# Performance work log

Hardware: AMD Instinct MI355X
Metric: run time of the kernel (lower is better)

The kernel has to match this reference:

```python
import jax, jax.numpy as jnp
import numpy as np

H = 8  # attention_heads


def _ln(x, w, b, eps=1e-5):
    mu = x.mean(axis=-1, keepdims=True)
    var = x.var(axis=-1, keepdims=True)
    return (x - mu) / jnp.sqrt(var + eps) * w + b


def setup_inputs() -> dict:
    key = jax.random.key(0)
    ks = jax.random.split(key, 10)
    B, T, C, U, D, P = 4, 256, 2048, 4, 512, 512
    s = 0.02
    inp = {
        "model_embed": jax.random.normal(ks[0], (B, T, D), jnp.float32),
        "context_embed_key": jax.random.normal(ks[1], (C, U, D), jnp.float32),
        "context_embed_value": jax.random.normal(ks[2], (C, D), jnp.float32),
        "ln1_w": jnp.ones((D,), jnp.float32), "ln1_b": jnp.zeros((D,), jnp.float32),
        "ln2_w": jnp.ones((D,), jnp.float32), "ln2_b": jnp.zeros((D,), jnp.float32),
        "ln3_w": jnp.ones((D,), jnp.float32), "ln3_b": jnp.zeros((D,), jnp.float32),
        "ln4_w": jnp.ones((D,), jnp.float32), "ln4_b": jnp.zeros((D,), jnp.float32),
        "wq": jax.random.normal(ks[3], (D, D), jnp.float32) * s, "bq": jnp.zeros((D,), jnp.float32),
        "wk": jax.random.normal(ks[4], (D, D), jnp.float32) * s, "bk": jnp.zeros((D,), jnp.float32),
        "wv": jax.random.normal(ks[5], (D, D), jnp.float32) * s, "bv": jnp.zeros((D,), jnp.float32),
        "wo": jax.random.normal(ks[6], (D, D), jnp.float32) * s, "bo": jnp.zeros((D,), jnp.float32),
        "wp": jax.random.normal(ks[7], (D, P), jnp.float32) * s, "bp": jnp.zeros((P,), jnp.float32),
    }
    return inp


def reference(model_embed, context_embed_key, context_embed_value,
              ln1_w, ln1_b, ln2_w, ln2_b, ln3_w, ln3_b, ln4_w, ln4_b,
              wq, bq, wk, bk, wv, bv, wo, bo, wp, bp):
    B, T, D = model_embed.shape
    C, U, _ = context_embed_key.shape
    dk = D // H
    # pre-attention LayerNorms (norm_before_x1/x2/x3)
    q = _ln(model_embed, ln1_w, ln1_b)
    k = _ln(context_embed_key, ln2_w, ln2_b)
    v = _ln(context_embed_value, ln3_w, ln3_b)
    # q/k/v projections, split heads
    q = (q @ wq + bq).reshape(B, T, H, dk)
    k = (k @ wk + bk).reshape(C, U, H, dk)
    v = (v @ wv + bv).reshape(C, H, dk)
    # ColBERT late interaction: score every query token against every
    # context vector, MaxSim over the U vectors of each context entry.
    scores = jnp.einsum('bthd,cuhd->bhtcu', q, k) / jnp.sqrt(jnp.asarray(dk, q.dtype))
    scores = scores.max(axis=-1)                 # [B,H,T,C]
    attn = jax.nn.softmax(scores, axis=-1)       # softmax over contexts C
    out = jnp.einsum('bhtc,chd->bthd', attn, v).reshape(B, T, D)
    out = out @ wo + bo                          # attention output proj
    out = _ln(out, ln4_w, ln4_b)                 # norm_after
    return out @ wp + bp                         # final proj -> [B,T,P]
```

## Files before the change

### kernel.cpp

```cpp
#include <hip/hip_runtime.h>
#include <hip/hip_bf16.h>

using bf16 = __hip_bfloat16;

#define D_DIM 512
#define C_DIM 2048
#define U_DIM 4
#define DK 64

typedef __attribute__((ext_vector_type(8))) short short8;
typedef __attribute__((ext_vector_type(8))) unsigned short ushort8;
typedef __attribute__((ext_vector_type(4))) float f32x4;

__device__ __forceinline__ float dload(const void* p, size_t i, int f) {
    return f ? ((const float*)p)[i] : __bfloat162float(((const bf16*)p)[i]);
}
__device__ __forceinline__ unsigned f2bf(float x) {
    bf16 b = __float2bfloat16(x);
    return (unsigned)*(unsigned short*)&b;
}
__device__ __forceinline__ float bf2f(unsigned short us) {
    unsigned u = ((unsigned)us) << 16;
    return __builtin_bit_cast(float, u);
}

__device__ __forceinline__ int block_detect(const void* __restrict__ x) {
    __shared__ int sred[4];
    const bf16* xb = (const bf16*)x;
    int tid = threadIdx.x;
    int cnt = 0;
    #pragma unroll
    for (int i = 0; i < 4; ++i) {
        ushort8 a = *(const ushort8*)(xb + (size_t)(i * 256 + tid) * 8);
        #pragma unroll
        for (int j = 0; j < 8; ++j) {
            float v = fabsf(bf2f(a[j]));
            if (!(v <= 100.0f)) cnt++;
        }
    }
    #pragma unroll
    for (int o = 32; o > 0; o >>= 1) cnt += __shfl_down(cnt, o);
    if ((tid & 63) == 0) sred[tid >> 6] = cnt;
    __syncthreads();
    int c = sred[0] + sred[1] + sred[2] + sred[3];
    return (c > 400) ? 1 : 0;
}

template <bool LN, bool XF, bool WF>
__device__ __forceinline__ void pack_a_body(const void* __restrict__ X,
                                            const void* __restrict__ lnw,
                                            const void* __restrict__ lnb,
                                            uint4* __restrict__ Af, int tt) {
    int m = threadIdx.x >> 4;
    int kbL = threadIdx.x & 15;
    int row = tt * 16 + m;
    float v[32];
    float s = 0.0f, ss = 0.0f;
    #pragma unroll
    for (int i = 0; i < 4; ++i) {
        int k0 = (kbL + i * 16) * 8;
        if constexpr (XF) {
            const float4* p = (const float4*)((const float*)X + (size_t)row * D_DIM + k0);
            float4 a = p[0], b = p[1];
            v[i*8+0] = a.x; v[i*8+1] = a.y; v[i*8+2] = a.z; v[i*8+3] = a.w;
            v[i*8+4] = b.x; v[i*8+5] = b.y; v[i*8+6] = b.z; v[i*8+7] = b.w;
        } else {
            ushort8 a = *(const ushort8*)((const bf16*)X + (size_t)row * D_DIM + k0);
            #pragma unroll
            for (int j = 0; j < 8; ++j) v[i*8+j] = bf2f(a[j]);
        }
        #pragma unroll
        for (int j = 0; j < 8; ++j) { float x = v[i*8+j]; s += x; ss += x * x; }
    }
    float mu = 0.0f, rs = 1.0f;
    if (LN) {
        #pragma unroll
        for (int o = 1; o < 16; o <<= 1) { s += __shfl_xor(s, o); ss += __shfl_xor(ss, o); }
        mu = s * (1.0f / D_DIM);
        float var = ss * (1.0f / D_DIM) - mu * mu;
        rs = rsqrtf(var + 1e-5f);
    }
    #pragma unroll
    for (int i = 0; i < 4; ++i) {
        int kb = kbL + i * 16;
        int k0 = kb * 8;
        float lw[8], lb[8];
        if (LN) {
            if constexpr (WF) {
                const float4* pw = (const float4*)((const float*)lnw + k0);
                const float4* pb = (const float4*)((const float*)lnb + k0);
                float4 w0 = pw[0], w1 = pw[1], b0 = pb[0], b1 = pb[1];
                lw[0]=w0.x; lw[1]=w0.y; lw[2]=w0.z; lw[3]=w0.w;
                lw[4]=w1.x; lw[5]=w1.y; lw[6]=w1.z; lw[7]=w1.w;
                lb[0]=b0.x; lb[1]=b0.y; lb[2]=b0.z; lb[3]=b0.w;
                lb[4]=b1.x; lb[5]=b1.y; lb[6]=b1.z; lb[7]=b1.w;
            } else {
                ushort8 w8 = *(const ushort8*)((const bf16*)lnw + k0);
                ushort8 b8 = *(const ushort8*)((const bf16*)lnb + k0);
                #pragma unroll
                for (int j = 0; j < 8; ++j) { lw[j] = bf2f(w8[j]); lb[j] = bf2f(b8[j]); }
            }
        }
        unsigned pk[4];
        #pragma unroll
        for (int jp = 0; jp < 4; ++jp) {
            float v0 = v[i * 8 + jp * 2];
            float v1 = v[i * 8 + jp * 2 + 1];
            if (LN) {
                v0 = (v0 - mu) * rs * lw[jp * 2] + lb[jp * 2];
                v1 = (v1 - mu) * rs * lw[jp * 2 + 1] + lb[jp * 2 + 1];
            }
            pk[jp] = f2bf(v0) | (f2bf(v1) << 16);
        }
        uint4 wv = {pk[0], pk[1], pk[2], pk[3]};
        Af[((size_t)tt * 64 + kb) * 16 + m] = wv;
    }
}

template <bool WF>
__device__ __forceinline__ void pack_w_body(const void* __restrict__ W,
                                            uint4* __restrict__ Bf, int b,
                                            float (*t)[65]) {
    int n0 = (b & 7) * 64, k0 = (b >> 3) * 64;
    int tid = threadIdx.x;
    if constexpr (WF) {
        #pragma unroll
        for (int i = 0; i < 4; ++i) {
            int e = i * 256 + tid;
            int r = e >> 4, c = (e & 15) * 4;
            float4 a = *(const float4*)((const float*)W + (size_t)(k0 + r) * D_DIM + n0 + c);
            t[r][c] = a.x; t[r][c+1] = a.y; t[r][c+2] = a.z; t[r][c+3] = a.w;
        }
    } else {
        #pragma unroll
        for (int i = 0; i < 2; ++i) {
            int e = i * 256 + tid;
            int r = e >> 3, c = (e & 7) * 8;
            ushort8 a = *(const ushort8*)((const bf16*)W + (size_t)(k0 + r) * D_DIM + n0 + c);
            #pragma unroll
            for (int j = 0; j < 8; ++j) t[r][c + j] = bf2f(a[j]);
        }
    }
    __syncthreads();
    #pragma unroll
    for (int i = 0; i < 2; ++i) {
        int e = i * 256 + tid;
        int nl = e & 63, kbl = e >> 6;
        unsigned pk[4];
        #pragma unroll
        for (int jp = 0; jp < 4; ++jp)
            pk[jp] = f2bf(t[kbl * 8 + jp * 2][nl]) | (f2bf(t[kbl * 8 + jp * 2 + 1][nl]) << 16);
        uint4 wv = {pk[0], pk[1], pk[2], pk[3]};
        int n = n0 + nl;
        Bf[(((size_t)(n >> 4)) * 64 + (k0 / 8 + kbl)) * 16 + (n & 15)] = wv;
    }
}

__global__ __launch_bounds__(256, 1)
void pack_all_kernel(const void* __restrict__ me, const void* __restrict__ l1w, const void* __restrict__ l1b,
                     const void* __restrict__ ck, const void* __restrict__ l2w, const void* __restrict__ l2b,
                     const void* __restrict__ cv, const void* __restrict__ l3w, const void* __restrict__ l3b,
                     uint4* __restrict__ Aq, uint4* __restrict__ Ak, uint4* __restrict__ Av,
                     const void* W0, const void* W1, const void* W2,
                     const void* W3, const void* W4,
                     uint4* B0, uint4* B1, uint4* B2, uint4* B3, uint4* B4,
                     int* __restrict__ flagp) {
    __shared__ float t[64][65];
    int f = block_detect(me);
    if (blockIdx.x == 0 && threadIdx.x == 0) *flagp = f;
    int b = blockIdx.x;
    const void* Ws[5] = {W0, W1, W2, W3, W4};
    uint4* Bs[5] = {B0, B1, B2, B3, B4};
    if (f) {
        if (b < 64)       pack_a_body<true, true, true>(me, l1w, l1b, Aq, b);
        else if (b < 576) pack_a_body<true, true, true>(ck, l2w, l2b, Ak, b - 64);
        else if (b < 704) pack_a_body<true, true, true>(cv, l3w, l3b, Av, b - 576);
        else { int c = b - 704; pack_w_body<true>(Ws[c >> 6], Bs[c >> 6], c & 63, t); }
    } else {
        if (b < 64)       pack_a_body<true, false, false>(me, l1w, l1b, Aq, b);
        else if (b < 576) pack_a_body<true, false, false>(ck, l2w, l2b, Ak, b - 64);
        else if (b < 704) pack_a_body<true, false, false>(cv, l3w, l3b, Av, b - 576);
        else { int c = b - 704; pack_w_body<false>(Ws[c >> 6], Bs[c >> 6], c & 63, t); }
    }
}

template <int OUT>
__device__ __forceinline__ void mfma_gemm_body(const uint4* __restrict__ Af,
                                               const uint4* __restrict__ Bf,
                                               const void* __restrict__ bias,
                                               uint4* __restrict__ Fout, int Rtt,
                                               int f, int bx, int by,
                                               float (*t)[65]) {
    int w = threadIdx.x >> 6, lane = threadIdx.x & 63;
    int q = lane >> 4, mn = lane & 15;
    int mt = by * 4 + w;
    int nt0 = bx * 4;
    f32x4 acc[4] = {{0.f,0.f,0.f,0.f},{0.f,0.f,0.f,0.f},{0.f,0.f,0.f,0.f},{0.f,0.f,0.f,0.f}};
    for (int kw = 0; kw < 16; ++kw) {
        short8 a = *(const short8*)(Af + ((size_t)mt * 64 + kw * 4 + q) * 16 + mn);
        #pragma unroll
        for (int i = 0; i < 4; ++i) {
            short8 b = *(const short8*)(Bf + (((size_t)(nt0 + i)) * 64 + kw * 4 + q) * 16 + mn);
            acc[i] = __builtin_amdgcn_mfma_f32_16x16x32_bf16(a, b, acc[i], 0, 0, 0);
        }
    }
    #pragma unroll
    for (int i = 0; i < 4; ++i) {
        float bv = dload(bias, (nt0 + i) * 16 + mn, f);
        #pragma unroll
        for (int r = 0; r < 4; ++r)
            t[w * 16 + q * 4 + r][i * 16 + mn] = acc[i][r] + bv;
    }
    __syncthreads();
    int h = bx;
    if constexpr (OUT == 1) {
        #pragma unroll
        for (int e0 = 0; e0 < 2; ++e0) {
            int e = e0 * 256 + threadIdx.x;
            int m = e & 15, kb = (e >> 4) & 7, ttl = e >> 7;
            const float* src = &t[ttl * 16 + m][kb * 8];
            uint4 wv;
            wv.x = f2bf(src[0]) | (f2bf(src[1]) << 16);
            wv.y = f2bf(src[2]) | (f2bf(src[3]) << 16);
            wv.z = f2bf(src[4]) | (f2bf(src[5]) << 16);
            wv.w = f2bf(src[6]) | (f2bf(src[7]) << 16);
            Fout[(((size_t)h * Rtt + by * 4 + ttl) * 8 + kb) * 16 + m] = wv;
        }
    } else if constexpr (OUT == 2) {
        #pragma unroll
        for (int e0 = 0; e0 < 2; ++e0) {
            int e = e0 * 256 + threadIdx.x;
            int lane2 = e & 63, nt = (e >> 6) & 3, ctl = e >> 8;
            int nm2 = lane2 & 15, q2 = lane2 >> 4;
            int col = nt * 16 + nm2;
            int rb = ctl * 32 + q2 * 8;
            uint4 wv;
            wv.x = f2bf(t[rb + 0][col]) | (f2bf(t[rb + 1][col]) << 16);
            wv.y = f2bf(t[rb + 2][col]) | (f2bf(t[rb + 3][col]) << 16);
            wv.z = f2bf(t[rb + 4][col]) | (f2bf(t[rb + 5][col]) << 16);
            wv.w = f2bf(t[rb + 6][col]) | (f2bf(t[rb + 7][col]) << 16);
            Fout[(((size_t)h * 64 + by * 2 + ctl) * 4 + nt) * 64 + lane2] = wv;
        }
    } else {
        #pragma unroll
        for (int e0 = 0; e0 < 2; ++e0) {
            int e = e0 * 256 + threadIdx.x;
            int m2 = e & 15, kb = (e >> 4) & 7, u = e >> 7;
            const float* src = &t[m2 * 4 + u][kb * 8];
            uint4 wv;
            wv.x = f2bf(src[0]) | (f2bf(src[1]) << 16);
            wv.y = f2bf(src[2]) | (f2bf(src[3]) << 16);
            wv.z = f2bf(src[4]) | (f2bf(src[5]) << 16);
            wv.w = f2bf(src[6]) | (f2bf(src[7]) << 16);
            int nt = by * 4 + u;
            Fout[(((size_t)h * 512 + nt) * 8 + kb) * 16 + m2] = wv;
        }
    }
}

__global__ __launch_bounds__(256, 1)
void gemm_qkv_kernel(const uint4* __restrict__ Aq, const uint4* __restrict__ Ak,
                     const uint4* __restrict__ Av,
                     const uint4* __restrict__ wfq, const uint4* __restrict__ wfk,
                     const uint4* __restrict__ wfv,
                     const void* __restrict__ bq, const void* __restrict__ bk,
                     const void* __restrict__ bv,
                     uint4* __restrict__ qf, uint4* __restrict__ kf,
                     uint4* __restrict__ vf,
                     const int* __restrict__ flagp) {
    __shared__ float t[64][65];
    int f = *flagp;
    int b = blockIdx.x;
    if (b < 1024) {
        mfma_gemm_body<3>(Ak, wfk, bk, kf, 512, f, b >> 7, b & 127, t);
    } else if (b < 1280) {
        int c = b - 1024;
        mfma_gemm_body<2>(Av, wfv, bv, vf, 0, f, c >> 5, c & 31, t);
    } else {
        int c = b - 1280;
        mfma_gemm_body<1>(Aq, wfq, bq, qf, 64, f, c >> 4, c & 15, t);
    }
}

__global__ __launch_bounds__(256, 1)
void attn_fused_kernel(const uint4* __restrict__ qf, const uint4* __restrict__ kf,
                       const uint4* __restrict__ vf,
                       float* __restrict__ pacc, float* __restrict__ pm,
                       float* __restrict__ pl) {
    __shared__ float sp[4][16][36];
    int tid = threadIdx.x;
    int w = tid >> 6, lane = tid & 63;
    int q = lane >> 4, nm = lane & 15;
    int b = blockIdx.x;
    int h = b & 7;
    int s = (b >> 3) & 7;
    int qb = b >> 6;
    int mt = qb * 4 + w;

    short8 a0 = *(const short8*)(qf + (((size_t)h * 64 + mt) * 8 + q) * 16 + nm);
    short8 a1 = *(const short8*)(qf + (((size_t)h * 64 + mt) * 8 + 4 + q) * 16 + nm);

    f32x4 sc[8][2];
    #pragma unroll
    for (int st = 0; st < 8; ++st) {
        #pragma unroll
        for (int hh = 0; hh < 2; ++hh) {
            int ct16 = (s * 8 + st) * 2 + hh;
            f32x4 scv = {-1e30f, -1e30f, -1e30f, -1e30f};
            __builtin_amdgcn_s_setprio(1);
            #pragma unroll
            for (int u = 0; u < 4; ++u) {
                int nt = ct16 * 4 + u;
                short8 b0 = *(const short8*)(kf + (((size_t)h * 512 + nt) * 8 + q) * 16 + nm);
                short8 b1 = *(const short8*)(kf + (((size_t)h * 512 + nt) * 8 + 4 + q) * 16 + nm);
                f32x4 acc = {0.0f, 0.0f, 0.0f, 0.0f};
                acc = __builtin_amdgcn_mfma_f32_16x16x32_bf16(a0, b0, acc, 0, 0, 0);
                acc = __builtin_amdgcn_mfma_f32_16x16x32_bf16(a1, b1, acc, 0, 0, 0);
                #pragma unroll
                for (int r = 0; r < 4; ++r) scv[r] = fmaxf(scv[r], acc[r]);
            }
            __builtin_amdgcn_s_setprio(0);
            #pragma unroll
            for (int r = 0; r < 4; ++r) sc[st][hh][r] = scv[r] * 0.125f;
        }
    }

    float mrow[4], lrow[4];
    #pragma unroll
    for (int r = 0; r < 4; ++r) {
        float m = sc[0][0][r];
        #pragma unroll
        for (int st = 0; st < 8; ++st) {
            m = fmaxf(m, sc[st][0][r]);
            m = fmaxf(m, sc[st][1][r]);
        }
        m = fmaxf(m, __shfl_xor(m, 1));
        m = fmaxf(m, __shfl_xor(m, 2));
        m = fmaxf(m, __shfl_xor(m, 4));
        m = fmaxf(m, __shfl_xor(m, 8));
        mrow[r] = m;
        lrow[r] = 0.0f;
    }

    f32x4 acc_o[4] = {{0.f,0.f,0.f,0.f},{0.f,0.f,0.f,0.f},{0.f,0.f,0.f,0.f},{0.f,0.f,0.f,0.f}};
    #pragma unroll
    for (int st = 0; st < 8; ++st) {
        #pragma unroll
        for (int r = 0; r < 4; ++r) {
            float p0 = __expf(sc[st][0][r] - mrow[r]);
            float p1 = __expf(sc[st][1][r] - mrow[r]);
            sp[w][q * 4 + r][nm] = p0;
            sp[w][q * 4 + r][16 + nm] = p1;
            lrow[r] += p0 + p1;
        }
        float4 pa0 = *(const float4*)&sp[w][nm][q * 8];
        float4 pa1 = *(const float4*)&sp[w][nm][q * 8 + 4];
        uint4 av;
        av.x = f2bf(pa0.x) | (f2bf(pa0.y) << 16);
        av.y = f2bf(pa0.z) | (f2bf(pa0.w) << 16);
        av.z = f2bf(pa1.x) | (f2bf(pa1.y) << 16);
        av.w = f2bf(pa1.z) | (f2bf(pa1.w) << 16);
        short8 ap = *(short8*)&av;
        int ct32 = s * 8 + st;
        __builtin_amdgcn_s_setprio(1);
        #pragma unroll
        for (int nt2 = 0; nt2 < 4; ++nt2) {
            short8 bv = *(const short8*)(vf + (((size_t)h * 64 + ct32) * 4 + nt2) * 64 + lane);
            acc_o[nt2] = __builtin_amdgcn_mfma_f32_16x16x32_bf16(ap, bv, acc_o[nt2], 0, 0, 0);
        }
        __builtin_amdgcn_s_setprio(0);
    }

    #pragma unroll
    for (int r = 0; r < 4; ++r) {
        float ps = lrow[r];
        ps += __shfl_xor(ps, 1);
        ps += __shfl_xor(ps, 2);
        ps += __shfl_xor(ps, 4);
        ps += __shfl_xor(ps, 8);
        lrow[r] = ps;
    }

    int p_idx = ((qb * 8 + h) << 3) + s;
    float* po = pacc + ((size_t)p_idx * 64 + w * 16) * 64;
    #pragma unroll
    for (int nt2 = 0; nt2 < 4; ++nt2)
        #pragma unroll
        for (int r = 0; r < 4; ++r)
            po[(q * 4 + r) * 64 + nt2 * 16 + nm] = acc_o[nt2][r];
    if (nm == 0) {
        #pragma unroll
        for (int r = 0; r < 4; ++r) {
            pm[p_idx * 64 + w * 16 + q * 4 + r] = mrow[r];
            pl[p_idx * 64 + w * 16 + q * 4 + r] = lrow[r];
        }
    }
}

__global__ __launch_bounds__(256, 1)
void attn_merge_kernel(const float* __restrict__ pacc, const float* __restrict__ pm,
                       const float* __restrict__ pl, uint4* __restrict__ oAf) {
    int b = blockIdx.x;
    int g = b >> 1;
    int qb = g >> 3, h = g & 7;
    int tid = threadIdx.x;
    int r32 = tid >> 3, dg = tid & 7;
    int t_loc = (b & 1) * 32 + r32;
    int p0 = g * 8;
    float M = -1e30f;
    #pragma unroll
    for (int s = 0; s < 8; ++s) M = fmaxf(M, pm[(p0 + s) * 64 + t_loc]);
    float L = 0.0f;
    float4 o0 = {}, o1 = {};
    #pragma unroll
    for (int s = 0; s < 8; ++s) {
        float e = __expf(pm[(p0 + s) * 64 + t_loc] - M);
        L += pl[(p0 + s) * 64 + t_loc] * e;
        const float4* po = (const float4*)(pacc + ((size_t)(p0 + s) * 64 + t_loc) * 64 + dg * 8);
        float4 v0 = po[0], v1 = po[1];
        o0.x += v0.x * e; o0.y += v0.y * e; o0.z += v0.z * e; o0.w += v0.w * e;
        o1.x += v1.x * e; o1.y += v1.y * e; o1.z += v1.z * e; o1.w += v1.w * e;
    }
    float inv = 1.0f / L;
    int t = qb * 64 + t_loc;
    int tt = t >> 4, m = t & 15;
    int kb = h * 8 + dg;
    uint4 u;
    u.x = f2bf(o0.x * inv) | (f2bf(o0.y * inv) << 16);
    u.y = f2bf(o0.z * inv) | (f2bf(o0.w * inv) << 16);
    u.z = f2bf(o1.x * inv) | (f2bf(o1.y * inv) << 16);
    u.w = f2bf(o1.z * inv) | (f2bf(o1.w * inv) << 16);
    oAf[((size_t)tt * 64 + kb) * 16 + m] = u;
}

__global__ __launch_bounds__(512, 1)
void tail2_kernel(const uint4* __restrict__ oAf,
                  const uint4* __restrict__ wfo, const uint4* __restrict__ wfp,
                  const void* __restrict__ bo, const void* __restrict__ bp,
                  const void* __restrict__ ln4w, const void* __restrict__ ln4b,
                  float* __restrict__ Y, const int* __restrict__ flagp) {
    __shared__ uint4 lfr[64][16];
    __shared__ float xs[8][16][68];
    __shared__ float lw4[512], lb4[512];
    __shared__ float sred[8][16][2];
    int f = *flagp;
    int tid = threadIdx.x;
    int rt = blockIdx.x;
    if (tid < 512) { lw4[tid] = dload(ln4w, tid, f); lb4[tid] = dload(ln4b, tid, f); }

    int w = tid >> 6, lane = tid & 63;
    int q = lane >> 4, mn = lane & 15;

    f32x4 acc[4] = {{0.f,0.f,0.f,0.f},{0.f,0.f,0.f,0.f},{0.f,0.f,0.f,0.f},{0.f,0.f,0.f,0.f}};
    for (int kw = 0; kw < 16; ++kw) {
        short8 a = *(const short8*)(oAf + ((size_t)rt * 64 + kw * 4 + q) * 16 + mn);
        #pragma unroll
        for (int i = 0; i < 4; ++i) {
            int nt = w * 4 + i;
            short8 b = *(const short8*)(wfo + ((size_t)nt * 64 + kw * 4 + q) * 16 + mn);
            acc[i] = __builtin_amdgcn_mfma_f32_16x16x32_bf16(a, b, acc[i], 0, 0, 0);
        }
    }
    #pragma unroll
    for (int i = 0; i < 4; ++i) {
        float bv = dload(bo, (w * 4 + i) * 16 + mn, f);
        #pragma unroll
        for (int r = 0; r < 4; ++r) acc[i][r] += bv;
    }

    {
        float ps[4], pq[4];
        #pragma unroll
        for (int r = 0; r < 4; ++r) {
            float s = 0.f, sq = 0.f;
            #pragma unroll
            for (int i = 0; i < 4; ++i) { float x = acc[i][r]; s += x; sq += x * x; }
            #pragma unroll
            for (int o = 1; o < 16; o <<= 1) { s += __shfl_xor(s, o); sq += __shfl_xor(sq, o); }
            ps[r] = s; pq[r] = sq;
        }
        if (mn == 0) {
            #pragma unroll
            for (int r = 0; r < 4; ++r) { sred[w][q*4+r][0] = ps[r]; sred[w][q*4+r][1] = pq[r]; }
        }
    }
    __syncthreads();

    float mu[4], rs[4];
    #pragma unroll
    for (int r = 0; r < 4; ++r) {
        int rr = q * 4 + r;
        float s = 0.f, sq = 0.f;
        #pragma unroll
        for (int ww = 0; ww < 8; ++ww) { s += sred[ww][rr][0]; sq += sred[ww][rr][1]; }
        mu[r] = s * (1.0f / D_DIM);
        float var = sq * (1.0f / D_DIM) - mu[r] * mu[r];
        rs[r] = rsqrtf(var + 1e-5f);
    }

    #pragma unroll
    for (int i = 0; i < 4; ++i) {
        int col = w * 64 + i * 16 + mn;
        float g = lw4[col], bb = lb4[col];
        #pragma unroll
        for (int r = 0; r < 4; ++r) {
            float x = (acc[i][r] - mu[r]) * rs[r] * g + bb;
            xs[w][q * 4 + r][i * 16 + mn] = x;
        }
    }
    __syncthreads();

    #pragma unroll
    for (int it = 0; it < 2; ++it) {
        int idx = it * 64 + lane;
        int m = idx & 15, kbl = idx >> 4;
        const float* src = &xs[w][m][kbl * 8];
        float4 s0 = *(const float4*)src;
        float4 s1 = *(const float4*)(src + 4);
        uint4 u;
        u.x = f2bf(s0.x) | (f2bf(s0.y) << 16);
        u.y = f2bf(s0.z) | (f2bf(s0.w) << 16);
        u.z = f2bf(s1.x) | (f2bf(s1.y) << 16);
        u.w = f2bf(s1.z) | (f2bf(s1.w) << 16);
        lfr[w * 8 + kbl][m] = u;
    }
    __syncthreads();

    f32x4 acc2[4] = {{0.f,0.f,0.f,0.f},{0.f,0.f,0.f,0.f},{0.f,0.f,0.f,0.f},{0.f,0.f,0.f,0.f}};
    for (int kw = 0; kw < 16; ++kw) {
        short8 a = *(const short8*)&lfr[kw * 4 + q][mn];
        #pragma unroll
        for (int i = 0; i < 4; ++i) {
            int nt = w * 4 + i;
            short8 b = *(const short8*)(wfp + ((size_t)nt * 64 + kw * 4 + q) * 16 + mn);
            acc2[i] = __builtin_amdgcn_mfma_f32_16x16x32_bf16(a, b, acc2[i], 0, 0, 0);
        }
    }
    #pragma unroll
    for (int i = 0; i < 4; ++i) {
        int col = (w * 4 + i) * 16 + mn;
        float bv = dload(bp, col, f);
        #pragma unroll
        for (int r = 0; r < 4; ++r)
            Y[(size_t)(rt * 16 + q * 4 + r) * D_DIM + col] = acc2[i][r] + bv;
    }
}

extern "C" void kernel_launch(void* const* d_in, const int* in_sizes, int n_in,
                              void* d_out, int out_size, void* d_ws, size_t ws_size,
                              hipStream_t stream) {
    const void* model_embed = d_in[0];
    const void* ctx_key     = d_in[1];
    const void* ctx_val     = d_in[2];
    const void* ln1w = d_in[3];  const void* ln1b = d_in[4];
    const void* ln2w = d_in[5];  const void* ln2b = d_in[6];
    const void* ln3w = d_in[7];  const void* ln3b = d_in[8];
    const void* ln4w = d_in[9];  const void* ln4b = d_in[10];
    const void* wq = d_in[11];   const void* bq = d_in[12];
    const void* wk = d_in[13];   const void* bk = d_in[14];
    const void* wv = d_in[15];   const void* bv = d_in[16];
    const void* wo = d_in[17];   const void* bo = d_in[18];
    const void* wp = d_in[19];   const void* bp = d_in[20];

    int*   flagp = (int*)d_ws;
    float* ws    = (float*)d_ws + 16;
    float* o1    = ws;
    float* qTf   = o1 + 524288;
    float* kTf   = qTf + 262144;
    float* Aqf   = kTf + 2097152;
    float* Akf   = Aqf + 262144;
    float* Avf   = Akf + 2097152;
    float* vff   = Avf + 524288;
    float* pacc2 = vff + 524288;
    float* pm2   = pacc2 + 4194304;
    float* pl2   = pm2 + 65536;
    float* wfr   = pl2 + 65536;

    uint4* qf  = (uint4*)qTf;
    uint4* kf  = (uint4*)kTf;
    uint4* Aq  = (uint4*)Aqf;
    uint4* Ak  = (uint4*)Akf;
    uint4* Av  = (uint4*)Avf;
    uint4* vf  = (uint4*)vff;
    uint4* oAf = (uint4*)o1;
    uint4* wfq = (uint4*)wfr;
    uint4* wfk = wfq + 32768;
    uint4* wfv = wfk + 32768;
    uint4* wfo = wfv + 32768;
    uint4* wfp = wfo + 32768;

    pack_all_kernel<<<1024, 256, 0, stream>>>(model_embed, ln1w, ln1b,
                                              ctx_key, ln2w, ln2b,
                                              ctx_val, ln3w, ln3b,
                                              Aq, Ak, Av,
                                              wq, wk, wv, wo, wp,
                                              wfq, wfk, wfv, wfo, wfp, flagp);

    gemm_qkv_kernel<<<1408, 256, 0, stream>>>(Aq, Ak, Av, wfq, wfk, wfv,
                                              bq, bk, bv, qf, kf, vf, flagp);

    attn_fused_kernel<<<1024, 256, 0, stream>>>(qf, kf, vf, pacc2, pm2, pl2);

    attn_merge_kernel<<<256, 256, 0, stream>>>(pacc2, pm2, pl2, oAf);

    tail2_kernel<<<64, 512, 0, stream>>>(oAf, wfo, wfp, bo, bp,
                                         ln4w, ln4b, (float*)d_out, flagp);

    (void)ws_size;
}
```

Baseline: 185.9 us.

## Fuse split-context attention merge into attention kernel via shared memory

Each attention block now holds 8 waves, one per context split, working on a single 16-row query tile for one head. Partial outputs and softmax statistics go to LDS instead of global memory, and the block merges them before writing the bf16 result. This removes the separate merge kernel launch and a large global round trip of partial accumulators. In exchange, each block covers fewer query rows, so K/V reuse across query tiles inside a block is lost, and most threads sit idle during the merge. Separately, the QKV GEMM launch bound is raised to allow two blocks per CU.

Measured after the change: 182.2 us. 1.02x faster.

```diff
diff --git a/kernel.cpp b/kernel.cpp
--- a/kernel.cpp
+++ b/kernel.cpp
@@ -258,7 +258,7 @@
     }
 }
 
-__global__ __launch_bounds__(256, 1)
+__global__ __launch_bounds__(256, 2)
 void gemm_qkv_kernel(const uint4* __restrict__ Aq, const uint4* __restrict__ Ak,
                      const uint4* __restrict__ Av,
                      const uint4* __restrict__ wfq, const uint4* __restrict__ wfk,
@@ -282,23 +282,23 @@
     }
 }
 
-__global__ __launch_bounds__(256, 1)
+__global__ __launch_bounds__(512, 1)
 void attn_fused_kernel(const uint4* __restrict__ qf, const uint4* __restrict__ kf,
-                       const uint4* __restrict__ vf,
-                       float* __restrict__ pacc, float* __restrict__ pm,
-                       float* __restrict__ pl) {
-    __shared__ float sp[4][16][36];
+                       const uint4* __restrict__ vf, uint4* __restrict__ oAf) {
+    __shared__ float sp[8][16][36];
+    __shared__ float opar[8][16][64];
+    __shared__ float mpar[8][16];
+    __shared__ float lpar[8][16];
     int tid = threadIdx.x;
     int w = tid >> 6, lane = tid & 63;
     int q = lane >> 4, nm = lane & 15;
     int b = blockIdx.x;
     int h = b & 7;
-    int s = (b >> 3) & 7;
-    int qb = b >> 6;
-    int mt = qb * 4 + w;
-
-    short8 a0 = *(const short8*)(qf + (((size_t)h * 64 + mt) * 8 + q) * 16 + nm);
-    short8 a1 = *(const short8*)(qf + (((size_t)h * 64 + mt) * 8 + 4 + q) * 16 + nm);
+    int rt = b >> 3;
+    int s = w;
+
+    short8 a0 = *(const short8*)(qf + (((size_t)h * 64 + rt) * 8 + q) * 16 + nm);
+    short8 a1 = *(const short8*)(qf + (((size_t)h * 64 + rt) * 8 + 4 + q) * 16 + nm);
 
     f32x4 sc[8][2];
     #pragma unroll
@@ -381,56 +381,44 @@
         lrow[r] = ps;
     }
 
-    int p_idx = ((qb * 8 + h) << 3) + s;
-    float* po = pacc + ((size_t)p_idx * 64 + w * 16) * 64;
     #pragma unroll
     for (int nt2 = 0; nt2 < 4; ++nt2)
         #pragma unroll
         for (int r = 0; r < 4; ++r)
-            po[(q * 4 + r) * 64 + nt2 * 16 + nm] = acc_o[nt2][r];
+            opar[w][q * 4 + r][nt2 * 16 + nm] = acc_o[nt2][r];
     if (nm == 0) {
         #pragma unroll
         for (int r = 0; r < 4; ++r) {
-            pm[p_idx * 64 + w * 16 + q * 4 + r] = mrow[r];
-            pl[p_idx * 64 + w * 16 + q * 4 + r] = lrow[r];
-        }
-    }
-}
-
-__global__ __launch_bounds__(256, 1)
-void attn_merge_kernel(const float* __restrict__ pacc, const float* __restrict__ pm,
-                       const float* __restrict__ pl, uint4* __restrict__ oAf) {
-    int b = blockIdx.x;
-    int g = b >> 1;
-    int qb = g >> 3, h = g & 7;
-    int tid = threadIdx.x;
-    int r32 = tid >> 3, dg = tid & 7;
-    int t_loc = (b & 1) * 32 + r32;
-    int p0 = g * 8;
-    float M = -1e30f;
-    #pragma unroll
-    for (int s = 0; s < 8; ++s) M = fmaxf(M, pm[(p0 + s) * 64 + t_loc]);
-    float L = 0.0f;
-    float4 o0 = {}, o1 = {};
-    #pragma unroll
-    for (int s = 0; s < 8; ++s) {
-        float e = __expf(pm[(p0 + s) * 64 + t_loc] - M);
-        L += pl[(p0 + s) * 64 + t_loc] * e;
-        const float4* po = (const float4*)(pacc + ((size_t)(p0 + s) * 64 + t_loc) * 64 + dg * 8);
-        float4 v0 = po[0], v1 = po[1];
-        o0.x += v0.x * e; o0.y += v0.y * e; o0.z += v0.z * e; o0.w += v0.w * e;
-        o1.x += v1.x * e; o1.y += v1.y * e; o1.z += v1.z * e; o1.w += v1.w * e;
-    }
-    float inv = 1.0f / L;
-    int t = qb * 64 + t_loc;
-    int tt = t >> 4, m = t & 15;
-    int kb = h * 8 + dg;
-    uint4 u;
-    u.x = f2bf(o0.x * inv) | (f2bf(o0.y * inv) << 16);
-    u.y = f2bf(o0.z * inv) | (f2bf(o0.w * inv) << 16);
-    u.z = f2bf(o1.x * inv) | (f2bf(o1.y * inv) << 16);
-    u.w = f2bf(o1.z * inv) | (f2bf(o1.w * inv) << 16);
-    oAf[((size_t)tt * 64 + kb) * 16 + m] = u;
+            mpar[w][q * 4 + r] = mrow[r];
+            lpar[w][q * 4 + r] = lrow[r];
+        }
+    }
+    __syncthreads();
+
+    if (tid < 128) {
+        int row = tid & 15, dg = tid >> 4;
+        float M = -1e30f;
+        #pragma unroll
+        for (int ss = 0; ss < 8; ++ss) M = fmaxf(M, mpar[ss][row]);
+        float L = 0.0f;
+        float o[8] = {0.f,0.f,0.f,0.f,0.f,0.f,0.f,0.f};
+        #pragma unroll
+        for (int ss = 0; ss < 8; ++ss) {
+            float e = __expf(mpar[ss][row] - M);
+            L += lpar[ss][row] * e;
+            const float* po = &opar[ss][row][dg * 8];
+            #pragma unroll
+            for (int j = 0; j < 8; ++j) o[j] += po[j] * e;
+        }
+        float inv = 1.0f / L;
+        uint4 u;
+        u.x = f2bf(o[0] * inv) | (f2bf(o[1] * inv) << 16);
+        u.y = f2bf(o[2] * inv) | (f2bf(o[3] * inv) << 16);
+        u.z = f2bf(o[4] * inv) | (f2bf(o[5] * inv) << 16);
+        u.w = f2bf(o[6] * inv) | (f2bf(o[7] * inv) << 16);
+        int kb = h * 8 + dg;
+        oAf[((size_t)rt * 64 + kb) * 16 + row] = u;
+    }
 }
 
 __global__ __launch_bounds__(512, 1)
@@ -571,10 +559,7 @@
     float* Akf   = Aqf + 262144;
     float* Avf   = Akf + 2097152;
     float* vff   = Avf + 524288;
-    float* pacc2 = vff + 524288;
-    float* pm2   = pacc2 + 4194304;
-    float* pl2   = pm2 + 65536;
-    float* wfr   = pl2 + 65536;
+    float* wfr   = vff + 524288;
 
     uint4* qf  = (uint4*)qTf;
     uint4* kf  = (uint4*)kTf;
@@ -599,9 +584,7 @@
     gemm_qkv_kernel<<<1408, 256, 0, stream>>>(Aq, Ak, Av, wfq, wfk, wfv,
                                               bq, bk, bv, qf, kf, vf, flagp);
 
-    attn_fused_kernel<<<1024, 256, 0, stream>>>(qf, kf, vf, pacc2, pm2, pl2);
-
-    attn_merge_kernel<<<256, 256, 0, stream>>>(pacc2, pm2, pl2, oAf);
+    attn_fused_kernel<<<512, 512, 0, stream>>>(qf, kf, vf, oAf);
 
     tail2_kernel<<<64, 512, 0, stream>>>(oAf, wfo, wfp, bo, bp,
                                          ln4w, ln4b, (float*)d_out, flagp);
```
